# Kernel optimization log

Hardware: AMD Instinct MI355X
Metric: run time of the kernel (lower is better)

## Reference

```python
import jax, jax.numpy as jnp
import numpy as np

# dims
N, E, B, T = 1024, 8192, 4, 8          # nodes, edges, batch, time steps
IN, HID, H, NCLASS = 64, 64, 4, 7      # in_dim, nhidden, heads, nclass
K = N - NCLASS + 1                     # output-head conv width
NEG, EPS = 0.2, 1e-5


def setup_inputs() -> dict:
    key = jax.random.key(0)
    ks = jax.random.split(key, 24)
    p = lambda i, shape: jax.random.normal(ks[i], shape, jnp.float32) * 0.05
    inputs = jax.random.normal(ks[0], (B, IN, T, N), jnp.float32)
    src = jax.random.randint(ks[1], (E,), 0, N, jnp.int32)
    dst = jnp.repeat(jnp.arange(N, dtype=jnp.int32), E // N)  # every node has in-degree 8
    return {
        "inputs": inputs, "src": src, "dst": dst,
        "W0": p(2, (H * HID, IN)), "al0": p(3, (H, HID)), "ar0": p(4, (H, HID)),
        "W1": p(5, (H * HID, H * HID)), "al1": p(6, (H, HID)), "ar1": p(7, (H, HID)),
        "W2": p(8, (H * 1, H * HID)), "al2": p(9, (H, 1)), "ar2": p(10, (H, 1)),
        "Wres2": p(11, (H * 1, H * HID)),
        # Outputlayer
        "tc1_w": p(12, (H, H, T)), "tc1_b": p(13, (H,)),
        "ln1_g": jnp.ones((N, H), jnp.float32), "ln1_b": jnp.zeros((N, H), jnp.float32),
        "tc2_w": p(14, (1, H)), "tc2_b": p(15, (1,)),
        "ln2_g": jnp.ones((N, 1), jnp.float32), "ln2_b": jnp.zeros((N, 1), jnp.float32),
        "fc_w": p(16, (K,)), "fc_b": p(17, (1,)),
    }


def _gat_conv(h, src, dst, W, al, ar, res=None, act=None):
    # h: (N,B,T,F) -> feat: (N,B,T,H,D)
    heads, d = al.shape
    feat = (h @ W.T).reshape(N, B, T, heads, d)
    el = jnp.einsum('nbthd,hd->nbth', feat, al)
    er = jnp.einsum('nbthd,hd->nbth', feat, ar)
    e = jax.nn.leaky_relu(el[src] + er[dst], NEG)           # (E,B,T,H)
    emax = jax.ops.segment_max(e, dst, num_segments=N)
    ex = jnp.exp(e - emax[dst])
    den = jax.ops.segment_sum(ex, dst, num_segments=N)
    a = ex / den[dst]                                        # edge softmax over incoming edges
    out = jax.ops.segment_sum(feat[src] * a[..., None], dst, num_segments=N)  # (N,B,T,H,D)
    if res is not None:
        out = out + res
    if act is not None:
        out = act(out)
    return out


def reference(inputs, src, dst,
              W0, al0, ar0, W1, al1, ar1, W2, al2, ar2, Wres2,
              tc1_w, tc1_b, ln1_g, ln1_b, tc2_w, tc2_b, ln2_g, ln2_b, fc_w, fc_b):
    # (B,IN,T,N) -> (N,B,T,IN) : transpose(0,3).transpose(1,3)
    h = jnp.transpose(inputs.astype(jnp.float32), (3, 0, 2, 1))
    h1 = _gat_conv(h, src, dst, W0, al0, ar0, act=jax.nn.elu).reshape(N, B, T, H * HID)
    h2 = _gat_conv(h1, src, dst, W1, al1, ar1,
                   res=h1.reshape(N, B, T, H, HID), act=jax.nn.elu).reshape(N, B, T, H * HID)
    res2 = (h2 @ Wres2.T).reshape(N, B, T, H, 1)
    o = _gat_conv(h2, src, dst, W2, al2, ar2, res=res2)      # (N,B,T,H,1)
    # transpose(1,3).transpose(0,3).squeeze(-1) -> (B,H,T,N)
    x = jnp.transpose(o[..., 0], (1, 3, 2, 0))

    # Outputlayer
    # tconv1: Conv2d(H->H, kernel (T,1)) collapses time -> (B,H,N)
    x1 = jnp.einsum('oht,bhtn->bon', tc1_w, x) + tc1_b[None, :, None]
    # ln1: LayerNorm over (N,H) of (B,1,N,H)
    z = jnp.transpose(x1, (0, 2, 1))                          # (B,N,H)
    mu = z.mean(axis=(1, 2), keepdims=True)
    var = z.var(axis=(1, 2), keepdims=True)
    z = (z - mu) / jnp.sqrt(var + EPS) * ln1_g + ln1_b
    x1 = jnp.transpose(z, (0, 2, 1))                          # (B,H,N)
    # tconv2: 1x1 conv H->1 -> (B,1,N)
    x2 = jnp.einsum('oh,bhn->bon', tc2_w, x1) + tc2_b[None, :, None]
    # ln2: LayerNorm over (N,1)
    mu = x2.mean(axis=2, keepdims=True)
    var = x2.var(axis=2, keepdims=True)
    x2 = (x2 - mu) / jnp.sqrt(var + EPS) * ln2_g[:, 0] + ln2_b[:, 0]
    # fc: Conv2d(1->1, kernel (1,K)) sliding over nodes -> (B,NCLASS)
    xc = x2[:, :, None, :]                                    # (B,1,1,N) NCHW
    w = fc_w[None, None, None, :]                             # (1,1,1,K) OIHW
    out = jax.lax.conv_general_dilated(xc, w, (1, 1), 'VALID') + fc_b[None, :, None, None]
    return out[:, 0, 0, :]                                    # (B, NCLASS)
```

## Files before the change

### kernel.cpp

```cpp
#include <hip/hip_runtime.h>
#include <math.h>

#define NEGS 0.2f
#define EPSF 1e-5f

typedef short s16x8 __attribute__((ext_vector_type(8)));
typedef float f32x4 __attribute__((ext_vector_type(4)));

__device__ __forceinline__ float b2f(unsigned short u) {
  union { unsigned int i; float f; } v; v.i = ((unsigned int)u) << 16; return v.f;
}
__device__ __forceinline__ unsigned short f2b(float f) {
  union { float f; unsigned int i; } v; v.f = f;
  unsigned int x = v.i;
  return (unsigned short)((x + 0x7fffu + ((x >> 16) & 1u)) >> 16);
}
__device__ __forceinline__ float elu_neg(float x) { return __expf(x) - 1.f; }

__device__ __forceinline__ void gbar(int* slot, int nb) {
  __syncthreads();
  if (threadIdx.x == 0) {
    int* cnt  = slot;
    int* flag = slot + 32;
    int old = __hip_atomic_fetch_add(cnt, 1, __ATOMIC_RELAXED, __HIP_MEMORY_SCOPE_AGENT);
    if (old == nb - 1) {
      __hip_atomic_store(flag, 1, __ATOMIC_RELEASE, __HIP_MEMORY_SCOPE_AGENT);
    } else {
      int it = 0;
      while (__hip_atomic_load(flag, __ATOMIC_RELAXED, __HIP_MEMORY_SCOPE_AGENT) == 0) {
        __builtin_amdgcn_s_sleep(2);
        if (++it > (1 << 22)) break;
      }
    }
  }
  __syncthreads();
}

__global__ __launch_bounds__(256, 4) void k_mega(
    const float* __restrict__ inp, const int* __restrict__ src,
    const float* __restrict__ W0, const float* __restrict__ al0, const float* __restrict__ ar0,
    const float* __restrict__ W1, const float* __restrict__ al1, const float* __restrict__ ar1,
    const float* __restrict__ W2, const float* __restrict__ al2, const float* __restrict__ ar2,
    const float* __restrict__ Wr2, const float* __restrict__ tc1w,
    unsigned short* __restrict__ W1bX, unsigned short* __restrict__ feat0,
    unsigned short* __restrict__ feat1,
    float* __restrict__ el0, float* __restrict__ er0,
    float* __restrict__ el1, float* __restrict__ er1,
    float* __restrict__ feat2, float* __restrict__ res2,
    float* __restrict__ x1, int* bar)
{
  __shared__ __align__(16) char pool[22528];
  const int tid = threadIdx.x;
  const int bid = blockIdx.x;
  const int g     = bid & 7;
  const int bt    = g*4 + ((bid >> 3) & 3);
  const int nBase = (bid >> 5) * 32;
  const int b = bt >> 3, t = bt & 7;
  const int w = tid >> 6, lane = tid & 63, n16 = lane & 15, q = lane >> 4;

  s16x8 h1r[2][2];

  {
    unsigned short (*At)[72] = (unsigned short(*)[72])pool;
    unsigned short *Lb = (unsigned short*)(pool + 4608);
    s16x8 bf[2][4];
    #pragma unroll
    for (int kc = 0; kc < 2; ++kc)
      #pragma unroll
      for (int ct = 0; ct < 4; ++ct) {
        const float* p = &W0[(size_t)((w*4 + ct)*16 + n16)*64 + kc*32 + q*8];
        float4 wa = *(const float4*)p;
        float4 wb = *(const float4*)(p + 4);
        s16x8 o;
        o[0]=(short)f2b(wa.x); o[1]=(short)f2b(wa.y); o[2]=(short)f2b(wa.z); o[3]=(short)f2b(wa.w);
        o[4]=(short)f2b(wb.x); o[5]=(short)f2b(wb.y); o[6]=(short)f2b(wb.z); o[7]=(short)f2b(wb.w);
        bf[kc][ct] = o;
      }
    {
      const int nn = tid & 31, cg = tid >> 5;
      #pragma unroll
      for (int c2 = 0; c2 < 4; ++c2) {
        const int ch = cg*8 + c2*2;
        float vx = inp[((size_t)(b*64 + ch  )*8 + t)*1024 + nBase + nn];
        float vy = inp[((size_t)(b*64 + ch+1)*8 + t)*1024 + nBase + nn];
        unsigned int pk = ((unsigned int)f2b(vy) << 16) | (unsigned int)f2b(vx);
        *(unsigned int*)&At[nn][ch] = pk;
      }
    }
    __syncthreads();
    f32x4 acc[2][4];
    #pragma unroll
    for (int rt = 0; rt < 2; ++rt)
      #pragma unroll
      for (int ct = 0; ct < 4; ++ct) acc[rt][ct] = (f32x4){0.f,0.f,0.f,0.f};
    #pragma unroll
    for (int kc = 0; kc < 2; ++kc) {
      s16x8 af[2];
      #pragma unroll
      for (int rt = 0; rt < 2; ++rt)
        af[rt] = *(const s16x8*)&At[rt*16 + n16][kc*32 + q*8];
      #pragma unroll
      for (int rt = 0; rt < 2; ++rt)
        #pragma unroll
        for (int ct = 0; ct < 4; ++ct)
          acc[rt][ct] = __builtin_amdgcn_mfma_f32_16x16x32_bf16(af[rt], bf[kc][ct], acc[rt][ct], 0, 0, 0);
    }
    float alv[4], arv[4];
    #pragma unroll
    for (int ct = 0; ct < 4; ++ct) {
      alv[ct] = al0[w*64 + ct*16 + n16];
      arv[ct] = ar0[w*64 + ct*16 + n16];
    }
    #pragma unroll
    for (int rt = 0; rt < 2; ++rt) {
      #pragma unroll
      for (int reg = 0; reg < 4; ++reg) {
        float pl = acc[rt][0][reg]*alv[0] + acc[rt][1][reg]*alv[1]
                 + acc[rt][2][reg]*alv[2] + acc[rt][3][reg]*alv[3];
        float pr = acc[rt][0][reg]*arv[0] + acc[rt][1][reg]*arv[1]
                 + acc[rt][2][reg]*arv[2] + acc[rt][3][reg]*arv[3];
        #pragma unroll
        for (int o = 1; o < 16; o <<= 1) { pl += __shfl_xor(pl, o); pr += __shfl_xor(pr, o); }
        if (n16 == 0) {
          int r = (nBase + rt*16 + q*4 + reg)*32 + bt;
          el0[r*4 + w] = pl;
          er0[r*4 + w] = pr;
        }
      }
    }
    #pragma unroll
    for (int rt = 0; rt < 2; ++rt)
      #pragma unroll
      for (int ct = 0; ct < 4; ++ct)
        #pragma unroll
        for (int reg = 0; reg < 4; ++reg)
          Lb[(rt*16 + q*4 + reg)*256 + w*64 + ct*16 + n16] = f2b(acc[rt][ct][reg]);
    __syncthreads();
    #pragma unroll
    for (int i = 0; i < 4; ++i) {
      int u = tid + i*256;
      int m = u >> 5, off = (u & 31) * 8;
      *(s16x8*)&feat0[(size_t)((nBase + m)*32 + bt)*256 + off] = *(const s16x8*)&Lb[m*256 + off];
    }
    {
      const int j = ((bid >> 3) << 9) + tid*2;
      float2 wv2 = *(const float2*)&W1[j];
      W1bX[(size_t)g*65536 + j]     = f2b(wv2.x);
      W1bX[(size_t)g*65536 + j + 1] = f2b(wv2.y);
    }
  }
  gbar(bar + (0*8 + g)*64, 128);

  {
    float (*wsm)[8][4] = (float(*)[8][4])pool;
    int   (*ssm)[8]    = (int(*)[8])(pool + 4096);
    unsigned short *smbuf = (unsigned short*)(pool + 5120);
    unsigned short (*At)[264] = (unsigned short(*)[264])smbuf;
    unsigned short *Lb = smbuf;
    ((int*)ssm)[tid] = src[nBase*8 + tid];
    __syncthreads();
    if (tid < 128) {
      const int nl = tid >> 2, h = tid & 3;
      const int rn = (nBase + nl)*32 + bt;
      const float erv = er0[rn*4 + h];
      float e[8]; float mx = -1e30f;
      #pragma unroll
      for (int j = 0; j < 8; ++j) {
        float v = el0[(ssm[nl][j]*32 + bt)*4 + h] + erv;
        v = v >= 0.f ? v : NEGS * v;
        e[j] = v; mx = fmaxf(mx, v);
      }
      float den = 0.f;
      #pragma unroll
      for (int j = 0; j < 8; ++j) { e[j] = __expf(e[j] - mx); den += e[j]; }
      const float inv = 1.f / den;
      #pragma unroll
      for (int j = 0; j < 8; ++j) wsm[nl][j][h] = e[j] * inv;
    }
    __syncthreads();
    {
      const int hw2 = tid >> 5, l5 = tid & 31;
      const int c0 = l5 * 8, hh = l5 >> 3;
      #pragma unroll
      for (int p2 = 0; p2 < 2; ++p2) {
        const int nlA = p2*16 + hw2, nlB = nlA + 8;
        s16x8 vA[8], vB[8];
        #pragma unroll
        for (int j = 0; j < 8; ++j) {
          vA[j] = *(const s16x8*)&feat0[(size_t)(ssm[nlA][j]*32 + bt)*256 + c0];
          vB[j] = *(const s16x8*)&feat0[(size_t)(ssm[nlB][j]*32 + bt)*256 + c0];
        }
        asm volatile("" ::: "memory");
        float aA[8] = {0,0,0,0,0,0,0,0}, aB[8] = {0,0,0,0,0,0,0,0};
        #pragma unroll
        for (int j = 0; j < 8; ++j) {
          const float wA = wsm[nlA][j][hh], wB = wsm[nlB][j][hh];
          #pragma unroll
          for (int i = 0; i < 8; ++i) {
            aA[i] = fmaf(wA, b2f((unsigned short)vA[j][i]), aA[i]);
            aB[i] = fmaf(wB, b2f((unsigned short)vB[j][i]), aB[i]);
          }
        }
        s16x8 oA, oB;
        #pragma unroll
        for (int i = 0; i < 8; ++i) {
          float xA = aA[i] > 0.f ? aA[i] : elu_neg(aA[i]);
          float xB = aB[i] > 0.f ? aB[i] : elu_neg(aB[i]);
          oA[i] = (short)f2b(xA); oB[i] = (short)f2b(xB);
        }
        *(s16x8*)&At[nlA][c0] = oA;
        *(s16x8*)&At[nlB][c0] = oB;
        h1r[p2][0] = oA;
        h1r[p2][1] = oB;
      }
    }
    __syncthreads();
    f32x4 acc[2][4];
    #pragma unroll
    for (int rt = 0; rt < 2; ++rt)
      #pragma unroll
      for (int ct = 0; ct < 4; ++ct) acc[rt][ct] = (f32x4){0.f,0.f,0.f,0.f};
    const unsigned short* W1g = W1bX + (size_t)g*65536;
    #pragma unroll
    for (int kc = 0; kc < 8; ++kc) {
      s16x8 af[2], bfr[4];
      #pragma unroll
      for (int rt = 0; rt < 2; ++rt)
        af[rt] = *(const s16x8*)&At[rt*16 + n16][kc*32 + q*8];
      #pragma unroll
      for (int ct = 0; ct < 4; ++ct)
        bfr[ct] = *(const s16x8*)&W1g[(size_t)((w*4 + ct)*16 + n16)*256 + kc*32 + q*8];
      #pragma unroll
      for (int rt = 0; rt < 2; ++rt)
        #pragma unroll
        for (int ct = 0; ct < 4; ++ct)
          acc[rt][ct] = __builtin_amdgcn_mfma_f32_16x16x32_bf16(af[rt], bfr[ct], acc[rt][ct], 0, 0, 0);
    }
    float alv[4], arv[4];
    #pragma unroll
    for (int ct = 0; ct < 4; ++ct) {
      alv[ct] = al1[w*64 + ct*16 + n16];
      arv[ct] = ar1[w*64 + ct*16 + n16];
    }
    #pragma unroll
    for (int rt = 0; rt < 2; ++rt) {
      #pragma unroll
      for (int reg = 0; reg < 4; ++reg) {
        float pl = acc[rt][0][reg]*alv[0] + acc[rt][1][reg]*alv[1]
                 + acc[rt][2][reg]*alv[2] + acc[rt][3][reg]*alv[3];
        float pr = acc[rt][0][reg]*arv[0] + acc[rt][1][reg]*arv[1]
                 + acc[rt][2][reg]*arv[2] + acc[rt][3][reg]*arv[3];
        #pragma unroll
        for (int o = 1; o < 16; o <<= 1) { pl += __shfl_xor(pl, o); pr += __shfl_xor(pr, o); }
        if (n16 == 0) {
          int r = (nBase + rt*16 + q*4 + reg)*32 + bt;
          el1[r*4 + w] = pl;
          er1[r*4 + w] = pr;
        }
      }
    }
    __syncthreads();
    #pragma unroll
    for (int rt = 0; rt < 2; ++rt)
      #pragma unroll
      for (int ct = 0; ct < 4; ++ct)
        #pragma unroll
        for (int reg = 0; reg < 4; ++reg)
          Lb[(rt*16 + q*4 + reg)*256 + w*64 + ct*16 + n16] = f2b(acc[rt][ct][reg]);
    __syncthreads();
    #pragma unroll
    for (int i = 0; i < 4; ++i) {
      int u = tid + i*256;
      int row = u >> 5, off = (u & 31) * 8;
      *(s16x8*)&feat1[(size_t)((nBase + row)*32 + bt)*256 + off] = *(const s16x8*)&Lb[row*256 + off];
    }
  }
  gbar(bar + (1*8 + g)*64, 128);

  {
    float (*wsm)[8][4] = (float(*)[8][4])pool;
    int   (*ssm)[8]    = (int(*)[8])(pool + 4096);
    float (*Wp)[256]   = (float(*)[256])(pool + 5120);
    ((int*)ssm)[tid] = src[nBase*8 + tid];
    for (int j2 = tid; j2 < 2048; j2 += 256) {
      int o = j2 >> 8, k = j2 & 255;
      Wp[o][k] = (o < 4) ? W2[o*256 + k] : Wr2[(o-4)*256 + k];
    }
    __syncthreads();
    if (tid < 128) {
      const int nl = tid >> 2, h = tid & 3;
      const int rn = (nBase + nl)*32 + bt;
      const float erv = er1[rn*4 + h];
      float e[8]; float mx = -1e30f;
      #pragma unroll
      for (int j = 0; j < 8; ++j) {
        float v = el1[(ssm[nl][j]*32 + bt)*4 + h] + erv;
        v = v >= 0.f ? v : NEGS * v;
        e[j] = v; mx = fmaxf(mx, v);
      }
      float den = 0.f;
      #pragma unroll
      for (int j = 0; j < 8; ++j) { e[j] = __expf(e[j] - mx); den += e[j]; }
      const float inv = 1.f / den;
      #pragma unroll
      for (int j = 0; j < 8; ++j) wsm[nl][j][h] = e[j] * inv;
    }
    __syncthreads();
    const int hw2 = tid >> 5, l5 = tid & 31;
    const int c0 = l5 * 8, hh = l5 >> 3;
    #pragma unroll
    for (int p2 = 0; p2 < 2; ++p2) {
      const int nlA = p2*16 + hw2, nlB = nlA + 8;
      const int rnA = (nBase + nlA)*32 + bt, rnB = (nBase + nlB)*32 + bt;
      s16x8 vA[8], vB[8];
      const s16x8 rrA = h1r[p2][0], rrB = h1r[p2][1];
      #pragma unroll
      for (int j = 0; j < 8; ++j) {
        vA[j] = *(const s16x8*)&feat1[(size_t)(ssm[nlA][j]*32 + bt)*256 + c0];
        vB[j] = *(const s16x8*)&feat1[(size_t)(ssm[nlB][j]*32 + bt)*256 + c0];
      }
      asm volatile("" ::: "memory");
      float aA[8] = {0,0,0,0,0,0,0,0}, aB[8] = {0,0,0,0,0,0,0,0};
      #pragma unroll
      for (int j = 0; j < 8; ++j) {
        const float wA = wsm[nlA][j][hh], wB = wsm[nlB][j][hh];
        #pragma unroll
        for (int i = 0; i < 8; ++i) {
          aA[i] = fmaf(wA, b2f((unsigned short)vA[j][i]), aA[i]);
          aB[i] = fmaf(wB, b2f((unsigned short)vB[j][i]), aB[i]);
        }
      }
      #pragma unroll
      for (int i = 0; i < 8; ++i) {
        float xA = aA[i] + b2f((unsigned short)rrA[i]);
        float xB = aB[i] + b2f((unsigned short)rrB[i]);
        aA[i] = xA > 0.f ? xA : elu_neg(xA);
        aB[i] = xB > 0.f ? xB : elu_neg(xB);
      }
      #pragma unroll
      for (int o = 0; o < 8; ++o) {
        float4 wa = *(const float4*)&Wp[o][c0];
        float4 wb = *(const float4*)&Wp[o][c0 + 4];
        float pA = aA[0]*wa.x + aA[1]*wa.y + aA[2]*wa.z + aA[3]*wa.w
                 + aA[4]*wb.x + aA[5]*wb.y + aA[6]*wb.z + aA[7]*wb.w;
        float pB = aB[0]*wa.x + aB[1]*wa.y + aB[2]*wa.z + aB[3]*wa.w
                 + aB[4]*wb.x + aB[5]*wb.y + aB[6]*wb.z + aB[7]*wb.w;
        #pragma unroll
        for (int off = 1; off < 32; off <<= 1) {
          pA += __shfl_xor(pA, off);
          pB += __shfl_xor(pB, off);
        }
        if (l5 == 0) {
          if (o < 4) { feat2[rnA*4 + o] = pA; feat2[rnB*4 + o] = pB; }
          else       { res2[rnA*4 + (o-4)] = pA; res2[rnB*4 + (o-4)] = pB; }
        }
      }
    }
  }
  gbar(bar + (2*8 + g)*64, 128);

  {
    int (*ssm)[8] = (int(*)[8])(pool + 4096);
    if (tid < 128) {
      const int nl = tid >> 2, h = tid & 3;
      const int n = nBase + nl;
      const int rn = n*32 + bt;
      const float av = al2[h], rv = ar2[h];
      const float erv = feat2[rn*4 + h] * rv;
      float f[8], e[8]; float m = -1e30f;
      #pragma unroll
      for (int j = 0; j < 8; ++j) {
        f[j] = feat2[(ssm[nl][j]*32 + bt)*4 + h];
        float v = f[j]*av + erv;
        v = v >= 0.f ? v : NEGS * v;
        e[j] = v; m = fmaxf(m, v);
      }
      float den = 0.f, num = 0.f;
      #pragma unroll
      for (int j = 0; j < 8; ++j) { float ex = __expf(e[j]-m); den += ex; num = fmaf(ex, f[j], num); }
      const float os = num/den + res2[rn*4 + h];
      float po[4];
      #pragma unroll
      for (int o = 0; o < 4; ++o) po[o] = tc1w[(o*4 + h)*8 + t] * os;
      #pragma unroll
      for (int off = 1; off < 4; off <<= 1)
        #pragma unroll
        for (int o = 0; o < 4; ++o) po[o] += __shfl_xor(po[o], off);
      float v = (h==0) ? po[0] : (h==1) ? po[1] : (h==2) ? po[2] : po[3];
      atomicAdd(&x1[(b*4 + h)*1024 + n], v);
    }
  }
}

__global__ __launch_bounds__(256) void k_fin(
    const float* __restrict__ x1g, const float* __restrict__ tc1b,
    const float* __restrict__ ln1g, const float* __restrict__ ln1b,
    const float* __restrict__ tc2w, const float* __restrict__ tc2b,
    const float* __restrict__ ln2g, const float* __restrict__ ln2b,
    const float* __restrict__ fcw, const float* __restrict__ fcb,
    float* __restrict__ out)
{
  __shared__ __align__(16) float x1s[4][1024];
  __shared__ float x2s[1024];
  __shared__ float redA[4], redB[4];
  __shared__ float redC[4][7];
  const int bb = blockIdx.x, tid = threadIdx.x;
  const int wv = tid >> 6, lane = tid & 63;
  float s = 0.f, qq = 0.f;
  #pragma unroll
  for (int i = 0; i < 4; ++i) {
    const int n = tid + i*256;
    #pragma unroll
    for (int o = 0; o < 4; ++o) {
      float a = x1g[(bb*4 + o)*1024 + n] + tc1b[o];
      x1s[o][n] = a; s += a; qq += a*a;
    }
  }
  #pragma unroll
  for (int o = 32; o > 0; o >>= 1) { s += __shfl_down(s, o); qq += __shfl_down(qq, o); }
  if (lane == 0) { redA[wv] = s; redB[wv] = qq; }
  __syncthreads();
  const float S = redA[0]+redA[1]+redA[2]+redA[3];
  const float Q = redB[0]+redB[1]+redB[2]+redB[3];
  const float mu  = S * (1.f/4096.f);
  const float var = Q * (1.f/4096.f) - mu*mu;
  const float inv = rsqrtf(var + EPSF);
  const float tb = tc2b[0];
  const float r0 = tc2w[0], r1 = tc2w[1], r2 = tc2w[2], r3 = tc2w[3];
  float accv[4]; float s2 = 0.f, q2 = 0.f;
  #pragma unroll
  for (int i = 0; i < 4; ++i) {
    const int n = tid + i*256;
    float4 g4 = *(const float4*)&ln1g[n*4];
    float4 b4 = *(const float4*)&ln1b[n*4];
    float a = tb;
    a = fmaf(r0, (x1s[0][n]-mu)*inv*g4.x + b4.x, a);
    a = fmaf(r1, (x1s[1][n]-mu)*inv*g4.y + b4.y, a);
    a = fmaf(r2, (x1s[2][n]-mu)*inv*g4.z + b4.z, a);
    a = fmaf(r3, (x1s[3][n]-mu)*inv*g4.w + b4.w, a);
    accv[i] = a; s2 += a; q2 += a*a;
  }
  __syncthreads();
  #pragma unroll
  for (int o = 32; o > 0; o >>= 1) { s2 += __shfl_down(s2, o); q2 += __shfl_down(q2, o); }
  if (lane == 0) { redA[wv] = s2; redB[wv] = q2; }
  __syncthreads();
  const float S2 = redA[0]+redA[1]+redA[2]+redA[3];
  const float Q2 = redB[0]+redB[1]+redB[2]+redB[3];
  const float mu2  = S2 * (1.f/1024.f);
  const float inv2 = rsqrtf(Q2 * (1.f/1024.f) - mu2*mu2 + EPSF);
  #pragma unroll
  for (int i = 0; i < 4; ++i) {
    const int n = tid + i*256;
    x2s[n] = (accv[i] - mu2) * inv2 * ln2g[n] + ln2b[n];
  }
  __syncthreads();
  float pc[7] = {0.f,0.f,0.f,0.f,0.f,0.f,0.f};
  for (int k = tid; k < 1018; k += 256) {
    const float fw = fcw[k];
    #pragma unroll
    for (int c = 0; c < 7; ++c) pc[c] = fmaf(x2s[k + c], fw, pc[c]);
  }
  #pragma unroll
  for (int o = 32; o > 0; o >>= 1)
    #pragma unroll
    for (int c = 0; c < 7; ++c) pc[c] += __shfl_down(pc[c], o);
  if (lane == 0) {
    #pragma unroll
    for (int c = 0; c < 7; ++c) redC[wv][c] = pc[c];
  }
  __syncthreads();
  if (tid < 7)
    out[bb*7 + tid] = redC[0][tid] + redC[1][tid] + redC[2][tid] + redC[3][tid] + fcb[0];
}

extern "C" void kernel_launch(void* const* d_in, const int* in_sizes, int n_in,
                              void* d_out, int out_size, void* d_ws, size_t ws_size,
                              hipStream_t stream)
{
  const float* inp  = (const float*)d_in[0];
  const int*   src  = (const int*)  d_in[1];
  const float* W0   = (const float*)d_in[3];
  const float* al0  = (const float*)d_in[4];
  const float* ar0  = (const float*)d_in[5];
  const float* W1   = (const float*)d_in[6];
  const float* al1  = (const float*)d_in[7];
  const float* ar1  = (const float*)d_in[8];
  const float* W2   = (const float*)d_in[9];
  const float* al2  = (const float*)d_in[10];
  const float* ar2  = (const float*)d_in[11];
  const float* Wr2  = (const float*)d_in[12];
  const float* tc1w = (const float*)d_in[13];
  const float* tc1b = (const float*)d_in[14];
  const float* ln1g = (const float*)d_in[15];
  const float* ln1b = (const float*)d_in[16];
  const float* tc2w = (const float*)d_in[17];
  const float* tc2b = (const float*)d_in[18];
  const float* ln2g = (const float*)d_in[19];
  const float* ln2b = (const float*)d_in[20];
  const float* fcw  = (const float*)d_in[21];
  const float* fcb  = (const float*)d_in[22];
  float* out = (float*)d_out;

  unsigned short* W1bX   = (unsigned short*)d_ws;
  unsigned short* featb0 = W1bX   + 524288;
  unsigned short* featb1 = featb0 + 8388608;
  float* el0   = (float*)(featb1 + 8388608);
  float* er0   = el0   + 131072;
  float* el1   = er0   + 131072;
  float* er1   = el1   + 131072;
  float* feat2 = er1   + 131072;
  float* res2  = feat2 + 131072;
  float* x1    = res2  + 131072;
  int*   bar   = (int*)(x1 + 16384);

  hipMemsetAsync(x1, 0, 16384*4 + 6144, stream);
  k_mega<<<dim3(1024), dim3(256), 0, stream>>>(inp, src, W0, al0, ar0, W1, al1, ar1,
                                               W2, al2, ar2, Wr2, tc1w,
                                               W1bX, featb0, featb1,
                                               el0, er0, el1, er1, feat2, res2, x1, bar);
  k_fin<<<dim3(4), dim3(256), 0, stream>>>(x1, tc1b, ln1g, ln1b, tc2w, tc2b,
                                           ln2g, ln2b, fcw, fcb, out);
}
```

Before: 173.2 us.

## Halve per-block node tile, double grid, use hierarchical grid barrier

Each block now handles 16 nodes instead of 32, so the persistent megakernel launches 2048 blocks with launch bounds raised to 8 blocks per CU and half the shared memory. The grid barrier is split into four sub-counters of 64 arrivals that feed a master counter, so fewer blocks contend on one atomic address. The aim is more resident waves to hide gather latency and cheaper barrier arrival. The risks are that all 2048 blocks must be co-resident for the spin barrier to avoid deadlock, and that W1 fragments are reloaded twice as often relative to the work done per block.

```diff
diff --git a/kernel.cpp b/kernel.cpp
--- a/kernel.cpp
+++ b/kernel.cpp
@@ -17,26 +17,25 @@
 }
 __device__ __forceinline__ float elu_neg(float x) { return __expf(x) - 1.f; }
 
-__device__ __forceinline__ void gbar(int* slot, int nb) {
+__device__ __forceinline__ void gbar(int* slot, int sub) {
   __syncthreads();
   if (threadIdx.x == 0) {
-    int* cnt  = slot;
-    int* flag = slot + 32;
-    int old = __hip_atomic_fetch_add(cnt, 1, __ATOMIC_RELAXED, __HIP_MEMORY_SCOPE_AGENT);
-    if (old == nb - 1) {
-      __hip_atomic_store(flag, 1, __ATOMIC_RELEASE, __HIP_MEMORY_SCOPE_AGENT);
-    } else {
-      int it = 0;
-      while (__hip_atomic_load(flag, __ATOMIC_RELAXED, __HIP_MEMORY_SCOPE_AGENT) == 0) {
-        __builtin_amdgcn_s_sleep(2);
-        if (++it > (1 << 22)) break;
-      }
-    }
-  }
-  __syncthreads();
-}
-
-__global__ __launch_bounds__(256, 4) void k_mega(
+    int old = __hip_atomic_fetch_add(slot + sub*16, 1, __ATOMIC_RELAXED, __HIP_MEMORY_SCOPE_AGENT);
+    if (old == 63) {
+      int om = __hip_atomic_fetch_add(slot + 64, 1, __ATOMIC_RELAXED, __HIP_MEMORY_SCOPE_AGENT);
+      if (om == 3)
+        __hip_atomic_store(slot + 96, 1, __ATOMIC_RELEASE, __HIP_MEMORY_SCOPE_AGENT);
+    }
+    int it = 0;
+    while (__hip_atomic_load(slot + 96, __ATOMIC_RELAXED, __HIP_MEMORY_SCOPE_AGENT) == 0) {
+      __builtin_amdgcn_s_sleep(2);
+      if (++it > (1 << 22)) break;
+    }
+  }
+  __syncthreads();
+}
+
+__global__ __launch_bounds__(256, 8) void k_mega(
     const float* __restrict__ inp, const int* __restrict__ src,
     const float* __restrict__ W0, const float* __restrict__ al0, const float* __restrict__ ar0,
     const float* __restrict__ W1, const float* __restrict__ al1, const float* __restrict__ ar1,
@@ -49,20 +48,21 @@
     float* __restrict__ feat2, float* __restrict__ res2,
     float* __restrict__ x1, int* bar)
 {
-  __shared__ __align__(16) char pool[22528];
+  __shared__ __align__(16) char pool[11264];
   const int tid = threadIdx.x;
   const int bid = blockIdx.x;
   const int g     = bid & 7;
   const int bt    = g*4 + ((bid >> 3) & 3);
-  const int nBase = (bid >> 5) * 32;
+  const int nBase = (bid >> 5) * 16;
+  const int sub   = (bid >> 3) & 3;
   const int b = bt >> 3, t = bt & 7;
   const int w = tid >> 6, lane = tid & 63, n16 = lane & 15, q = lane >> 4;
 
-  s16x8 h1r[2][2];
+  s16x8 h1r[2];
 
   {
     unsigned short (*At)[72] = (unsigned short(*)[72])pool;
-    unsigned short *Lb = (unsigned short*)(pool + 4608);
+    unsigned short *Lb = (unsigned short*)(pool + 2304);
     s16x8 bf[2][4];
     #pragma unroll
     for (int kc = 0; kc < 2; ++kc)
@@ -77,10 +77,10 @@
         bf[kc][ct] = o;
       }
     {
-      const int nn = tid & 31, cg = tid >> 5;
-      #pragma unroll
-      for (int c2 = 0; c2 < 4; ++c2) {
-        const int ch = cg*8 + c2*2;
+      const int nn = tid & 15, cg = tid >> 4;
+      #pragma unroll
+      for (int c2 = 0; c2 < 2; ++c2) {
+        const int ch = cg*4 + c2*2;
         float vx = inp[((size_t)(b*64 + ch  )*8 + t)*1024 + nBase + nn];
         float vy = inp[((size_t)(b*64 + ch+1)*8 + t)*1024 + nBase + nn];
         unsigned int pk = ((unsigned int)f2b(vy) << 16) | (unsigned int)f2b(vx);
@@ -88,22 +88,15 @@
       }
     }
     __syncthreads();
-    f32x4 acc[2][4];
-    #pragma unroll
-    for (int rt = 0; rt < 2; ++rt)
-      #pragma unroll
-      for (int ct = 0; ct < 4; ++ct) acc[rt][ct] = (f32x4){0.f,0.f,0.f,0.f};
+    f32x4 acc[4];
+    #pragma unroll
+    for (int ct = 0; ct < 4; ++ct) acc[ct] = (f32x4){0.f,0.f,0.f,0.f};
     #pragma unroll
     for (int kc = 0; kc < 2; ++kc) {
-      s16x8 af[2];
-      #pragma unroll
-      for (int rt = 0; rt < 2; ++rt)
-        af[rt] = *(const s16x8*)&At[rt*16 + n16][kc*32 + q*8];
-      #pragma unroll
-      for (int rt = 0; rt < 2; ++rt)
-        #pragma unroll
-        for (int ct = 0; ct < 4; ++ct)
-          acc[rt][ct] = __builtin_amdgcn_mfma_f32_16x16x32_bf16(af[rt], bf[kc][ct], acc[rt][ct], 0, 0, 0);
+      s16x8 af = *(const s16x8*)&At[n16][kc*32 + q*8];
+      #pragma unroll
+      for (int ct = 0; ct < 4; ++ct)
+        acc[ct] = __builtin_amdgcn_mfma_f32_16x16x32_bf16(af, bf[kc][ct], acc[ct], 0, 0, 0);
     }
     float alv[4], arv[4];
     #pragma unroll
@@ -112,54 +105,47 @@
       arv[ct] = ar0[w*64 + ct*16 + n16];
     }
     #pragma unroll
-    for (int rt = 0; rt < 2; ++rt) {
-      #pragma unroll
-      for (int reg = 0; reg < 4; ++reg) {
-        float pl = acc[rt][0][reg]*alv[0] + acc[rt][1][reg]*alv[1]
-                 + acc[rt][2][reg]*alv[2] + acc[rt][3][reg]*alv[3];
-        float pr = acc[rt][0][reg]*arv[0] + acc[rt][1][reg]*arv[1]
-                 + acc[rt][2][reg]*arv[2] + acc[rt][3][reg]*arv[3];
-        #pragma unroll
-        for (int o = 1; o < 16; o <<= 1) { pl += __shfl_xor(pl, o); pr += __shfl_xor(pr, o); }
-        if (n16 == 0) {
-          int r = (nBase + rt*16 + q*4 + reg)*32 + bt;
-          el0[r*4 + w] = pl;
-          er0[r*4 + w] = pr;
-        }
-      }
-    }
-    #pragma unroll
-    for (int rt = 0; rt < 2; ++rt)
-      #pragma unroll
-      for (int ct = 0; ct < 4; ++ct)
-        #pragma unroll
-        for (int reg = 0; reg < 4; ++reg)
-          Lb[(rt*16 + q*4 + reg)*256 + w*64 + ct*16 + n16] = f2b(acc[rt][ct][reg]);
-    __syncthreads();
-    #pragma unroll
-    for (int i = 0; i < 4; ++i) {
+    for (int reg = 0; reg < 4; ++reg) {
+      float pl = acc[0][reg]*alv[0] + acc[1][reg]*alv[1]
+               + acc[2][reg]*alv[2] + acc[3][reg]*alv[3];
+      float pr = acc[0][reg]*arv[0] + acc[1][reg]*arv[1]
+               + acc[2][reg]*arv[2] + acc[3][reg]*arv[3];
+      #pragma unroll
+      for (int o = 1; o < 16; o <<= 1) { pl += __shfl_xor(pl, o); pr += __shfl_xor(pr, o); }
+      if (n16 == 0) {
+        int r = (nBase + q*4 + reg)*32 + bt;
+        el0[r*4 + w] = pl;
+        er0[r*4 + w] = pr;
+      }
+    }
+    #pragma unroll
+    for (int ct = 0; ct < 4; ++ct)
+      #pragma unroll
+      for (int reg = 0; reg < 4; ++reg)
+        Lb[(q*4 + reg)*256 + w*64 + ct*16 + n16] = f2b(acc[ct][reg]);
+    __syncthreads();
+    #pragma unroll
+    for (int i = 0; i < 2; ++i) {
       int u = tid + i*256;
       int m = u >> 5, off = (u & 31) * 8;
       *(s16x8*)&feat0[(size_t)((nBase + m)*32 + bt)*256 + off] = *(const s16x8*)&Lb[m*256 + off];
     }
     {
-      const int j = ((bid >> 3) << 9) + tid*2;
-      float2 wv2 = *(const float2*)&W1[j];
-      W1bX[(size_t)g*65536 + j]     = f2b(wv2.x);
-      W1bX[(size_t)g*65536 + j + 1] = f2b(wv2.y);
-    }
-  }
-  gbar(bar + (0*8 + g)*64, 128);
+      const int k = bid >> 3;
+      W1bX[(size_t)g*65536 + k*256 + tid] = f2b(W1[k*256 + tid]);
+    }
+  }
+  gbar(bar + (0*8 + g)*128, sub);
 
   {
     float (*wsm)[8][4] = (float(*)[8][4])pool;
-    int   (*ssm)[8]    = (int(*)[8])(pool + 4096);
-    unsigned short *smbuf = (unsigned short*)(pool + 5120);
+    int   (*ssm)[8]    = (int(*)[8])(pool + 2048);
+    unsigned short *smbuf = (unsigned short*)(pool + 2560);
     unsigned short (*At)[264] = (unsigned short(*)[264])smbuf;
     unsigned short *Lb = smbuf;
-    ((int*)ssm)[tid] = src[nBase*8 + tid];
-    __syncthreads();
-    if (tid < 128) {
+    if (tid < 128) ((int*)ssm)[tid] = src[nBase*8 + tid];
+    __syncthreads();
+    if (tid < 64) {
       const int nl = tid >> 2, h = tid & 3;
       const int rn = (nBase + nl)*32 + bt;
       const float erv = er0[rn*4 + h];
@@ -181,60 +167,51 @@
     {
       const int hw2 = tid >> 5, l5 = tid & 31;
       const int c0 = l5 * 8, hh = l5 >> 3;
-      #pragma unroll
-      for (int p2 = 0; p2 < 2; ++p2) {
-        const int nlA = p2*16 + hw2, nlB = nlA + 8;
-        s16x8 vA[8], vB[8];
-        #pragma unroll
-        for (int j = 0; j < 8; ++j) {
-          vA[j] = *(const s16x8*)&feat0[(size_t)(ssm[nlA][j]*32 + bt)*256 + c0];
-          vB[j] = *(const s16x8*)&feat0[(size_t)(ssm[nlB][j]*32 + bt)*256 + c0];
-        }
-        asm volatile("" ::: "memory");
-        float aA[8] = {0,0,0,0,0,0,0,0}, aB[8] = {0,0,0,0,0,0,0,0};
-        #pragma unroll
-        for (int j = 0; j < 8; ++j) {
-          const float wA = wsm[nlA][j][hh], wB = wsm[nlB][j][hh];
-          #pragma unroll
-          for (int i = 0; i < 8; ++i) {
-            aA[i] = fmaf(wA, b2f((unsigned short)vA[j][i]), aA[i]);
-            aB[i] = fmaf(wB, b2f((unsigned short)vB[j][i]), aB[i]);
-          }
-        }
-        s16x8 oA, oB;
+      const int nlA = hw2, nlB = hw2 + 8;
+      s16x8 vA[8], vB[8];
+      #pragma unroll
+      for (int j = 0; j < 8; ++j) {
+        vA[j] = *(const s16x8*)&feat0[(size_t)(ssm[nlA][j]*32 + bt)*256 + c0];
+        vB[j] = *(const s16x8*)&feat0[(size_t)(ssm[nlB][j]*32 + bt)*256 + c0];
+      }
+      asm volatile("" ::: "memory");
+      float aA[8] = {0,0,0,0,0,0,0,0}, aB[8] = {0,0,0,0,0,0,0,0};
+      #pragma unroll
+      for (int j = 0; j < 8; ++j) {
+        const float wA = wsm[nlA][j][hh], wB = wsm[nlB][j][hh];
         #pragma unroll
         for (int i = 0; i < 8; ++i) {
-          float xA = aA[i] > 0.f ? aA[i] : elu_neg(aA[i]);
-          float xB = aB[i] > 0.f ? aB[i] : elu_neg(aB[i]);
-          oA[i] = (short)f2b(xA); oB[i] = (short)f2b(xB);
+          aA[i] = fmaf(wA, b2f((unsigned short)vA[j][i]), aA[i]);
+          aB[i] = fmaf(wB, b2f((unsigned short)vB[j][i]), aB[i]);
         }
-        *(s16x8*)&At[nlA][c0] = oA;
-        *(s16x8*)&At[nlB][c0] = oB;
-        h1r[p2][0] = oA;
-        h1r[p2][1] = oB;
-      }
-    }
-    __syncthreads();
-    f32x4 acc[2][4];
-    #pragma unroll
-    for (int rt = 0; rt < 2; ++rt)
-      #pragma unroll
-      for (int ct = 0; ct < 4; ++ct) acc[rt][ct] = (f32x4){0.f,0.f,0.f,0.f};
+      }
+      s16x8 oA, oB;
+      #pragma unroll
+      for (int i = 0; i < 8; ++i) {
+        float xA = aA[i] > 0.f ? aA[i] : elu_neg(aA[i]);
+        float xB = aB[i] > 0.f ? aB[i] : elu_neg(aB[i]);
+        oA[i] = (short)f2b(xA); oB[i] = (short)f2b(xB);
+      }
+      *(s16x8*)&At[nlA][c0] = oA;
+      *(s16x8*)&At[nlB][c0] = oB;
+      h1r[0] = oA;
+      h1r[1] = oB;
+    }
+    __syncthreads();
+    f32x4 acc[4];
+    #pragma unroll
+    for (int ct = 0; ct < 4; ++ct) acc[ct] = (f32x4){0.f,0.f,0.f,0.f};
     const unsigned short* W1g = W1bX + (size_t)g*65536;
     #pragma unroll
     for (int kc = 0; kc < 8; ++kc) {
-      s16x8 af[2], bfr[4];
-      #pragma unroll
-      for (int rt = 0; rt < 2; ++rt)
-        af[rt] = *(const s16x8*)&At[rt*16 + n16][kc*32 + q*8];
+      s16x8 af = *(const s16x8*)&At[n16][kc*32 + q*8];
+      s16x8 bfr[4];
       #pragma unroll
       for (int ct = 0; ct < 4; ++ct)
         bfr[ct] = *(const s16x8*)&W1g[(size_t)((w*4 + ct)*16 + n16)*256 + kc*32 + q*8];
       #pragma unroll
-      for (int rt = 0; rt < 2; ++rt)
-        #pragma unroll
-        for (int ct = 0; ct < 4; ++ct)
-          acc[rt][ct] = __builtin_amdgcn_mfma_f32_16x16x32_bf16(af[rt], bfr[ct], acc[rt][ct], 0, 0, 0);
+      for (int ct = 0; ct < 4; ++ct)
+        acc[ct] = __builtin_amdgcn_mfma_f32_16x16x32_bf16(af, bfr[ct], acc[ct], 0, 0, 0);
     }
     float alv[4], arv[4];
     #pragma unroll
@@ -243,51 +220,46 @@
       arv[ct] = ar1[w*64 + ct*16 + n16];
     }
     #pragma unroll
-    for (int rt = 0; rt < 2; ++rt) {
-      #pragma unroll
-      for (int reg = 0; reg < 4; ++reg) {
-        float pl = acc[rt][0][reg]*alv[0] + acc[rt][1][reg]*alv[1]
-                 + acc[rt][2][reg]*alv[2] + acc[rt][3][reg]*alv[3];
-        float pr = acc[rt][0][reg]*arv[0] + acc[rt][1][reg]*arv[1]
-                 + acc[rt][2][reg]*arv[2] + acc[rt][3][reg]*arv[3];
-        #pragma unroll
-        for (int o = 1; o < 16; o <<= 1) { pl += __shfl_xor(pl, o); pr += __shfl_xor(pr, o); }
-        if (n16 == 0) {
-          int r = (nBase + rt*16 + q*4 + reg)*32 + bt;
-          el1[r*4 + w] = pl;
-          er1[r*4 + w] = pr;
-        }
-      }
-    }
-    __syncthreads();
-    #pragma unroll
-    for (int rt = 0; rt < 2; ++rt)
-      #pragma unroll
-      for (int ct = 0; ct < 4; ++ct)
-        #pragma unroll
-        for (int reg = 0; reg < 4; ++reg)
-          Lb[(rt*16 + q*4 + reg)*256 + w*64 + ct*16 + n16] = f2b(acc[rt][ct][reg]);
-    __syncthreads();
-    #pragma unroll
-    for (int i = 0; i < 4; ++i) {
+    for (int reg = 0; reg < 4; ++reg) {
+      float pl = acc[0][reg]*alv[0] + acc[1][reg]*alv[1]
+               + acc[2][reg]*alv[2] + acc[3][reg]*alv[3];
+      float pr = acc[0][reg]*arv[0] + acc[1][reg]*arv[1]
+               + acc[2][reg]*arv[2] + acc[3][reg]*arv[3];
+      #pragma unroll
+      for (int o = 1; o < 16; o <<= 1) { pl += __shfl_xor(pl, o); pr += __shfl_xor(pr, o); }
+      if (n16 == 0) {
+        int r = (nBase + q*4 + reg)*32 + bt;
+        el1[r*4 + w] = pl;
+        er1[r*4 + w] = pr;
+      }
+    }
+    __syncthreads();
+    #pragma unroll
+    for (int ct = 0; ct < 4; ++ct)
+      #pragma unroll
+      for (int reg = 0; reg < 4; ++reg)
+        Lb[(q*4 + reg)*256 + w*64 + ct*16 + n16] = f2b(acc[ct][reg]);
+    __syncthreads();
+    #pragma unroll
+    for (int i = 0; i < 2; ++i) {
       int u = tid + i*256;
       int row = u >> 5, off = (u & 31) * 8;
       *(s16x8*)&feat1[(size_t)((nBase + row)*32 + bt)*256 + off] = *(const s16x8*)&Lb[row*256 + off];
     }
   }
-  gbar(bar + (1*8 + g)*64, 128);
+  gbar(bar + (1*8 + g)*128, sub);
 
   {
     float (*wsm)[8][4] = (float(*)[8][4])pool;
-    int   (*ssm)[8]    = (int(*)[8])(pool + 4096);
-    float (*Wp)[256]   = (float(*)[256])(pool + 5120);
-    ((int*)ssm)[tid] = src[nBase*8 + tid];
+    int   (*ssm)[8]    = (int(*)[8])(pool + 2048);
+    float (*Wp)[256]   = (float(*)[256])(pool + 2560);
+    if (tid < 128) ((int*)ssm)[tid] = src[nBase*8 + tid];
     for (int j2 = tid; j2 < 2048; j2 += 256) {
       int o = j2 >> 8, k = j2 & 255;
       Wp[o][k] = (o < 4) ? W2[o*256 + k] : Wr2[(o-4)*256 + k];
     }
     __syncthreads();
-    if (tid < 128) {
+    if (tid < 64) {
       const int nl = tid >> 2, h = tid & 3;
       const int rn = (nBase + nl)*32 + bt;
       const float erv = er1[rn*4 + h];
@@ -308,12 +280,11 @@
     __syncthreads();
     const int hw2 = tid >> 5, l5 = tid & 31;
     const int c0 = l5 * 8, hh = l5 >> 3;
-    #pragma unroll
-    for (int p2 = 0; p2 < 2; ++p2) {
-      const int nlA = p2*16 + hw2, nlB = nlA + 8;
+    {
+      const int nlA = hw2, nlB = hw2 + 8;
       const int rnA = (nBase + nlA)*32 + bt, rnB = (nBase + nlB)*32 + bt;
       s16x8 vA[8], vB[8];
-      const s16x8 rrA = h1r[p2][0], rrB = h1r[p2][1];
+      const s16x8 rrA = h1r[0], rrB = h1r[1];
       #pragma unroll
       for (int j = 0; j < 8; ++j) {
         vA[j] = *(const s16x8*)&feat1[(size_t)(ssm[nlA][j]*32 + bt)*256 + c0];
@@ -357,11 +328,11 @@
       }
     }
   }
-  gbar(bar + (2*8 + g)*64, 128);
+  gbar(bar + (2*8 + g)*128, sub);
 
   {
-    int (*ssm)[8] = (int(*)[8])(pool + 4096);
-    if (tid < 128) {
+    int (*ssm)[8] = (int(*)[8])(pool + 2048);
+    if (tid < 64) {
       const int nl = tid >> 2, h = tid & 3;
       const int n = nBase + nl;
       const int rn = n*32 + bt;
@@ -514,8 +485,8 @@
   float* x1    = res2  + 131072;
   int*   bar   = (int*)(x1 + 16384);
 
-  hipMemsetAsync(x1, 0, 16384*4 + 6144, stream);
-  k_mega<<<dim3(1024), dim3(256), 0, stream>>>(inp, src, W0, al0, ar0, W1, al1, ar1,
+  hipMemsetAsync(x1, 0, 16384*4 + 12288, stream);
+  k_mega<<<dim3(2048), dim3(256), 0, stream>>>(inp, src, W0, al0, ar0, W1, al1, ar1,
                                                W2, al2, ar2, Wr2, tc1w,
                                                W1bX, featb0, featb1,
                                                el0, er0, el1, er1, feat2, res2, x1, bar);
```

Result: slower. 365.3 us (+110.9%).

## Use hierarchical grid barrier, hoist gathers above softmax, load src indices once

Applied to the files above, without the earlier changes.

Replaces the flat 128-block atomic counter barrier with a two-level one: four sub-counters of 32 blocks each feed a master counter, and every block spins on a single flag. The first feature gather of the aggregation phases is issued before the edge-softmax computation and barrier so global loads overlap the attention work. Src indices are loaded into persistent shared memory once instead of once per phase. Input and W1 loads are widened to float4. In exchange it uses more barrier memory, adds register pressure from the hoisted vA/vB arrays, and the input transpose now writes single ushorts to shared memory, which may cause bank conflicts.

```diff
diff --git a/kernel.cpp b/kernel.cpp
--- a/kernel.cpp
+++ b/kernel.cpp
@@ -17,20 +17,19 @@
 }
 __device__ __forceinline__ float elu_neg(float x) { return __expf(x) - 1.f; }
 
-__device__ __forceinline__ void gbar(int* slot, int nb) {
+__device__ __forceinline__ void gbar(int* slot, int sub) {
   __syncthreads();
   if (threadIdx.x == 0) {
-    int* cnt  = slot;
-    int* flag = slot + 32;
-    int old = __hip_atomic_fetch_add(cnt, 1, __ATOMIC_RELAXED, __HIP_MEMORY_SCOPE_AGENT);
-    if (old == nb - 1) {
-      __hip_atomic_store(flag, 1, __ATOMIC_RELEASE, __HIP_MEMORY_SCOPE_AGENT);
-    } else {
-      int it = 0;
-      while (__hip_atomic_load(flag, __ATOMIC_RELAXED, __HIP_MEMORY_SCOPE_AGENT) == 0) {
-        __builtin_amdgcn_s_sleep(2);
-        if (++it > (1 << 22)) break;
-      }
+    int old = __hip_atomic_fetch_add(slot + sub*16, 1, __ATOMIC_RELAXED, __HIP_MEMORY_SCOPE_AGENT);
+    if (old == 31) {
+      int om = __hip_atomic_fetch_add(slot + 64, 1, __ATOMIC_RELAXED, __HIP_MEMORY_SCOPE_AGENT);
+      if (om == 3)
+        __hip_atomic_store(slot + 96, 1, __ATOMIC_RELEASE, __HIP_MEMORY_SCOPE_AGENT);
+    }
+    int it = 0;
+    while (__hip_atomic_load(slot + 96, __ATOMIC_RELAXED, __HIP_MEMORY_SCOPE_AGENT) == 0) {
+      __builtin_amdgcn_s_sleep(2);
+      if (++it > (1 << 22)) break;
     }
   }
   __syncthreads();
@@ -50,11 +49,13 @@
     float* __restrict__ x1, int* bar)
 {
   __shared__ __align__(16) char pool[22528];
+  int (*ssm)[8] = (int(*)[8])(pool + 21248);
   const int tid = threadIdx.x;
   const int bid = blockIdx.x;
   const int g     = bid & 7;
   const int bt    = g*4 + ((bid >> 3) & 3);
   const int nBase = (bid >> 5) * 32;
+  const int sub   = (bid >> 3) & 3;
   const int b = bt >> 3, t = bt & 7;
   const int w = tid >> 6, lane = tid & 63, n16 = lane & 15, q = lane >> 4;
 
@@ -63,6 +64,7 @@
   {
     unsigned short (*At)[72] = (unsigned short(*)[72])pool;
     unsigned short *Lb = (unsigned short*)(pool + 4608);
+    ((int*)ssm)[tid] = src[nBase*8 + tid];
     s16x8 bf[2][4];
     #pragma unroll
     for (int kc = 0; kc < 2; ++kc)
@@ -77,14 +79,15 @@
         bf[kc][ct] = o;
       }
     {
-      const int nn = tid & 31, cg = tid >> 5;
-      #pragma unroll
-      for (int c2 = 0; c2 < 4; ++c2) {
-        const int ch = cg*8 + c2*2;
-        float vx = inp[((size_t)(b*64 + ch  )*8 + t)*1024 + nBase + nn];
-        float vy = inp[((size_t)(b*64 + ch+1)*8 + t)*1024 + nBase + nn];
-        unsigned int pk = ((unsigned int)f2b(vy) << 16) | (unsigned int)f2b(vx);
-        *(unsigned int*)&At[nn][ch] = pk;
+      const int nn = tid & 7, cg = tid >> 3;
+      #pragma unroll
+      for (int c2 = 0; c2 < 2; ++c2) {
+        const int ch = cg + c2*32;
+        float4 v = *(const float4*)&inp[((size_t)(b*64 + ch)*8 + t)*1024 + nBase + nn*4];
+        At[nn*4 + 0][ch] = f2b(v.x);
+        At[nn*4 + 1][ch] = f2b(v.y);
+        At[nn*4 + 2][ch] = f2b(v.z);
+        At[nn*4 + 3][ch] = f2b(v.w);
       }
     }
     __syncthreads();
@@ -142,23 +145,28 @@
       int m = u >> 5, off = (u & 31) * 8;
       *(s16x8*)&feat0[(size_t)((nBase + m)*32 + bt)*256 + off] = *(const s16x8*)&Lb[m*256 + off];
     }
-    {
-      const int j = ((bid >> 3) << 9) + tid*2;
-      float2 wv2 = *(const float2*)&W1[j];
-      W1bX[(size_t)g*65536 + j]     = f2b(wv2.x);
-      W1bX[(size_t)g*65536 + j + 1] = f2b(wv2.y);
-    }
-  }
-  gbar(bar + (0*8 + g)*64, 128);
+    if (tid < 128) {
+      const int j = ((bid >> 3) << 9) + tid*4;
+      float4 w4 = *(const float4*)&W1[j];
+      ushort4 o4; o4.x=f2b(w4.x); o4.y=f2b(w4.y); o4.z=f2b(w4.z); o4.w=f2b(w4.w);
+      *(ushort4*)&W1bX[(size_t)g*65536 + j] = o4;
+    }
+  }
+  gbar(bar + (0*8 + g)*128, sub);
 
   {
     float (*wsm)[8][4] = (float(*)[8][4])pool;
-    int   (*ssm)[8]    = (int(*)[8])(pool + 4096);
-    unsigned short *smbuf = (unsigned short*)(pool + 5120);
+    unsigned short *smbuf = (unsigned short*)(pool + 4096);
     unsigned short (*At)[264] = (unsigned short(*)[264])smbuf;
     unsigned short *Lb = smbuf;
-    ((int*)ssm)[tid] = src[nBase*8 + tid];
-    __syncthreads();
+    const int hw2 = tid >> 5, l5 = tid & 31;
+    const int c0 = l5 * 8, hh = l5 >> 3;
+    s16x8 vA[8], vB[8];
+    #pragma unroll
+    for (int j = 0; j < 8; ++j) {
+      vA[j] = *(const s16x8*)&feat0[(size_t)(ssm[hw2    ][j]*32 + bt)*256 + c0];
+      vB[j] = *(const s16x8*)&feat0[(size_t)(ssm[hw2 + 8][j]*32 + bt)*256 + c0];
+    }
     if (tid < 128) {
       const int nl = tid >> 2, h = tid & 3;
       const int rn = (nBase + nl)*32 + bt;
@@ -178,41 +186,38 @@
       for (int j = 0; j < 8; ++j) wsm[nl][j][h] = e[j] * inv;
     }
     __syncthreads();
-    {
-      const int hw2 = tid >> 5, l5 = tid & 31;
-      const int c0 = l5 * 8, hh = l5 >> 3;
-      #pragma unroll
-      for (int p2 = 0; p2 < 2; ++p2) {
-        const int nlA = p2*16 + hw2, nlB = nlA + 8;
-        s16x8 vA[8], vB[8];
+    #pragma unroll
+    for (int p2 = 0; p2 < 2; ++p2) {
+      const int nlA = p2*16 + hw2, nlB = nlA + 8;
+      if (p2 == 1) {
         #pragma unroll
         for (int j = 0; j < 8; ++j) {
           vA[j] = *(const s16x8*)&feat0[(size_t)(ssm[nlA][j]*32 + bt)*256 + c0];
           vB[j] = *(const s16x8*)&feat0[(size_t)(ssm[nlB][j]*32 + bt)*256 + c0];
         }
-        asm volatile("" ::: "memory");
-        float aA[8] = {0,0,0,0,0,0,0,0}, aB[8] = {0,0,0,0,0,0,0,0};
-        #pragma unroll
-        for (int j = 0; j < 8; ++j) {
-          const float wA = wsm[nlA][j][hh], wB = wsm[nlB][j][hh];
-          #pragma unroll
-          for (int i = 0; i < 8; ++i) {
-            aA[i] = fmaf(wA, b2f((unsigned short)vA[j][i]), aA[i]);
-            aB[i] = fmaf(wB, b2f((unsigned short)vB[j][i]), aB[i]);
-          }
-        }
-        s16x8 oA, oB;
+      }
+      asm volatile("" ::: "memory");
+      float aA[8] = {0,0,0,0,0,0,0,0}, aB[8] = {0,0,0,0,0,0,0,0};
+      #pragma unroll
+      for (int j = 0; j < 8; ++j) {
+        const float wA = wsm[nlA][j][hh], wB = wsm[nlB][j][hh];
         #pragma unroll
         for (int i = 0; i < 8; ++i) {
-          float xA = aA[i] > 0.f ? aA[i] : elu_neg(aA[i]);
-          float xB = aB[i] > 0.f ? aB[i] : elu_neg(aB[i]);
-          oA[i] = (short)f2b(xA); oB[i] = (short)f2b(xB);
-        }
-        *(s16x8*)&At[nlA][c0] = oA;
-        *(s16x8*)&At[nlB][c0] = oB;
-        h1r[p2][0] = oA;
-        h1r[p2][1] = oB;
-      }
+          aA[i] = fmaf(wA, b2f((unsigned short)vA[j][i]), aA[i]);
+          aB[i] = fmaf(wB, b2f((unsigned short)vB[j][i]), aB[i]);
+        }
+      }
+      s16x8 oA, oB;
+      #pragma unroll
+      for (int i = 0; i < 8; ++i) {
+        float xA = aA[i] > 0.f ? aA[i] : elu_neg(aA[i]);
+        float xB = aB[i] > 0.f ? aB[i] : elu_neg(aB[i]);
+        oA[i] = (short)f2b(xA); oB[i] = (short)f2b(xB);
+      }
+      *(s16x8*)&At[nlA][c0] = oA;
+      *(s16x8*)&At[nlB][c0] = oB;
+      h1r[p2][0] = oA;
+      h1r[p2][1] = oB;
     }
     __syncthreads();
     f32x4 acc[2][4];
@@ -275,18 +280,21 @@
       *(s16x8*)&feat1[(size_t)((nBase + row)*32 + bt)*256 + off] = *(const s16x8*)&Lb[row*256 + off];
     }
   }
-  gbar(bar + (1*8 + g)*64, 128);
+  gbar(bar + (1*8 + g)*128, sub);
 
   {
     float (*wsm)[8][4] = (float(*)[8][4])pool;
-    int   (*ssm)[8]    = (int(*)[8])(pool + 4096);
-    float (*Wp)[256]   = (float(*)[256])(pool + 5120);
-    ((int*)ssm)[tid] = src[nBase*8 + tid];
-    for (int j2 = tid; j2 < 2048; j2 += 256) {
-      int o = j2 >> 8, k = j2 & 255;
-      Wp[o][k] = (o < 4) ? W2[o*256 + k] : Wr2[(o-4)*256 + k];
-    }
-    __syncthreads();
+    float (*Wp)[256]   = (float(*)[256])(pool + 4096);
+    const int hw2 = tid >> 5, l5 = tid & 31;
+    const int c0 = l5 * 8, hh = l5 >> 3;
+    s16x8 vA[8], vB[8];
+    #pragma unroll
+    for (int j = 0; j < 8; ++j) {
+      vA[j] = *(const s16x8*)&feat1[(size_t)(ssm[hw2    ][j]*32 + bt)*256 + c0];
+      vB[j] = *(const s16x8*)&feat1[(size_t)(ssm[hw2 + 8][j]*32 + bt)*256 + c0];
+    }
+    ((float4*)Wp)[tid]       = ((const float4*)W2)[tid & 255];
+    ((float4*)Wp)[256 + tid] = ((const float4*)Wr2)[tid & 255];
     if (tid < 128) {
       const int nl = tid >> 2, h = tid & 3;
       const int rn = (nBase + nl)*32 + bt;
@@ -306,20 +314,19 @@
       for (int j = 0; j < 8; ++j) wsm[nl][j][h] = e[j] * inv;
     }
     __syncthreads();
-    const int hw2 = tid >> 5, l5 = tid & 31;
-    const int c0 = l5 * 8, hh = l5 >> 3;
     #pragma unroll
     for (int p2 = 0; p2 < 2; ++p2) {
       const int nlA = p2*16 + hw2, nlB = nlA + 8;
       const int rnA = (nBase + nlA)*32 + bt, rnB = (nBase + nlB)*32 + bt;
-      s16x8 vA[8], vB[8];
+      if (p2 == 1) {
+        #pragma unroll
+        for (int j = 0; j < 8; ++j) {
+          vA[j] = *(const s16x8*)&feat1[(size_t)(ssm[nlA][j]*32 + bt)*256 + c0];
+          vB[j] = *(const s16x8*)&feat1[(size_t)(ssm[nlB][j]*32 + bt)*256 + c0];
+        }
+      }
+      asm volatile("" ::: "memory");
       const s16x8 rrA = h1r[p2][0], rrB = h1r[p2][1];
-      #pragma unroll
-      for (int j = 0; j < 8; ++j) {
-        vA[j] = *(const s16x8*)&feat1[(size_t)(ssm[nlA][j]*32 + bt)*256 + c0];
-        vB[j] = *(const s16x8*)&feat1[(size_t)(ssm[nlB][j]*32 + bt)*256 + c0];
-      }
-      asm volatile("" ::: "memory");
       float aA[8] = {0,0,0,0,0,0,0,0}, aB[8] = {0,0,0,0,0,0,0,0};
       #pragma unroll
       for (int j = 0; j < 8; ++j) {
@@ -357,38 +364,35 @@
       }
     }
   }
-  gbar(bar + (2*8 + g)*64, 128);
-
-  {
-    int (*ssm)[8] = (int(*)[8])(pool + 4096);
-    if (tid < 128) {
-      const int nl = tid >> 2, h = tid & 3;
-      const int n = nBase + nl;
-      const int rn = n*32 + bt;
-      const float av = al2[h], rv = ar2[h];
-      const float erv = feat2[rn*4 + h] * rv;
-      float f[8], e[8]; float m = -1e30f;
-      #pragma unroll
-      for (int j = 0; j < 8; ++j) {
-        f[j] = feat2[(ssm[nl][j]*32 + bt)*4 + h];
-        float v = f[j]*av + erv;
-        v = v >= 0.f ? v : NEGS * v;
-        e[j] = v; m = fmaxf(m, v);
-      }
-      float den = 0.f, num = 0.f;
-      #pragma unroll
-      for (int j = 0; j < 8; ++j) { float ex = __expf(e[j]-m); den += ex; num = fmaf(ex, f[j], num); }
-      const float os = num/den + res2[rn*4 + h];
-      float po[4];
-      #pragma unroll
-      for (int o = 0; o < 4; ++o) po[o] = tc1w[(o*4 + h)*8 + t] * os;
-      #pragma unroll
-      for (int off = 1; off < 4; off <<= 1)
-        #pragma unroll
-        for (int o = 0; o < 4; ++o) po[o] += __shfl_xor(po[o], off);
-      float v = (h==0) ? po[0] : (h==1) ? po[1] : (h==2) ? po[2] : po[3];
-      atomicAdd(&x1[(b*4 + h)*1024 + n], v);
-    }
+  gbar(bar + (2*8 + g)*128, sub);
+
+  if (tid < 128) {
+    const int nl = tid >> 2, h = tid & 3;
+    const int n = nBase + nl;
+    const int rn = n*32 + bt;
+    const float av = al2[h], rv = ar2[h];
+    const float erv = feat2[rn*4 + h] * rv;
+    float f[8], e[8]; float m = -1e30f;
+    #pragma unroll
+    for (int j = 0; j < 8; ++j) {
+      f[j] = feat2[(ssm[nl][j]*32 + bt)*4 + h];
+      float v = f[j]*av + erv;
+      v = v >= 0.f ? v : NEGS * v;
+      e[j] = v; m = fmaxf(m, v);
+    }
+    float den = 0.f, num = 0.f;
+    #pragma unroll
+    for (int j = 0; j < 8; ++j) { float ex = __expf(e[j]-m); den += ex; num = fmaf(ex, f[j], num); }
+    const float os = num/den + res2[rn*4 + h];
+    float po[4];
+    #pragma unroll
+    for (int o = 0; o < 4; ++o) po[o] = tc1w[(o*4 + h)*8 + t] * os;
+    #pragma unroll
+    for (int off = 1; off < 4; off <<= 1)
+      #pragma unroll
+      for (int o = 0; o < 4; ++o) po[o] += __shfl_xor(po[o], off);
+    float v = (h==0) ? po[0] : (h==1) ? po[1] : (h==2) ? po[2] : po[3];
+    atomicAdd(&x1[(b*4 + h)*1024 + n], v);
   }
 }
 
@@ -514,7 +518,7 @@
   float* x1    = res2  + 131072;
   int*   bar   = (int*)(x1 + 16384);
 
-  hipMemsetAsync(x1, 0, 16384*4 + 6144, stream);
+  hipMemsetAsync(x1, 0, 16384*4 + 12288, stream);
   k_mega<<<dim3(1024), dim3(256), 0, stream>>>(inp, src, W0, al0, ar0, W1, al1, ar1,
                                                W2, al2, ar2, Wr2, tc1w,
                                                W1bX, featb0, featb1,
```

New measurement: 178.7 us. +3.2%, slower.
